# Optimization experiments

Measured on AMD Instinct MI355X. Metric: run time of the kernel, lower is better.

Reference implementation:

```python
import jax, jax.numpy as jnp
import numpy as np
from jax import lax

B, T = 32, 20
H, E, A, V = 256, 512, 256, 10000
GH, GW, D = 32, 32, 256          # info spatial grid and channel dim
P = GH * GW                      # num_pixels = 1024
IN_FLAT = P * D                  # 262144
REL = 128 * 128                  # 16384
LSTM_IN = E + D + H              # input to gate linears (x = [word, att_feat], then cat h)


def setup_inputs() -> dict:
    key = jax.random.key(0)
    ks = iter(jax.random.split(key, 40))
    def W(shape, scale=0.05):
        return jax.random.normal(next(ks), shape, jnp.float32) * scale
    inp = {}
    inp["info"] = jax.random.normal(next(ks), (B, GH, GW, D), jnp.float32)
    inp["relation"] = jax.random.normal(next(ks), (B, 128, 128), jnp.float32)
    inp["captions"] = jax.random.randint(next(ks), (B, T), 0, V)
    lens = jax.random.randint(next(ks), (B, 1), 5, T + 1).at[0, 0].set(T)
    inp["captions_lens"] = lens
    # embedding + attention
    inp["emb"] = W((V, E), 0.1)
    inp["W_enc"] = W((D, A)); inp["b_enc"] = jnp.zeros((A,), jnp.float32)
    inp["W_dec"] = W((H, A)); inp["b_dec"] = jnp.zeros((A,), jnp.float32)
    inp["W_full"] = W((A,));  inp["b_full"] = jnp.zeros((), jnp.float32)
    # MSLSTM cell (5 gate linears + mlp)
    for g in ("i", "f", "o", "g1", "g2"):
        inp[f"W_{g}"] = W((LSTM_IN, H)); inp[f"b_{g}"] = jnp.zeros((H,), jnp.float32)
    inp["W_mlp"] = W((2 * H, H)); inp["b_mlp"] = jnp.zeros((H,), jnp.float32)
    # f_beta, fc, init-state linears
    inp["W_beta"] = W((H, D)); inp["b_beta"] = jnp.zeros((D,), jnp.float32)
    inp["W_fc"] = W((H, V), 0.1); inp["b_fc"] = jnp.zeros((V,), jnp.float32)
    inp["W_ih"] = W((IN_FLAT, H), 0.005); inp["b_ih"] = jnp.zeros((H,), jnp.float32)
    inp["W_ic"] = W((IN_FLAT, H), 0.005); inp["b_ic"] = jnp.zeros((H,), jnp.float32)
    inp["W_iC"] = W((REL, H), 0.01);      inp["b_iC"] = jnp.zeros((H,), jnp.float32)
    return inp


def reference(info, relation, captions, captions_lens, emb,
              W_enc, b_enc, W_dec, b_dec, W_full, b_full,
              W_i, b_i, W_f, b_f, W_o, b_o, W_g1, b_g1, W_g2, b_g2,
              W_mlp, b_mlp, W_beta, b_beta, W_fc, b_fc,
              W_ih, b_ih, W_ic, b_ic, W_iC, b_iC):
    Bsz = captions.shape[0]
    info_f = info.reshape(Bsz, P, D)
    rel_f = relation.reshape(Bsz, REL)
    lens = captions_lens[:, 0]
    order = jnp.argsort(-lens)                      # sort descending by length
    lens = lens[order]
    caps = captions[order]
    info_f = info_f[order]
    rel_f = rel_f[order]
    sent_len = lens - 1
    Tm = captions.shape[1] - 1                      # static: max len forced to T in setup

    words = emb[caps]                               # (B, T, E)
    flat = info_f.reshape(Bsz, -1)                  # (B, P*D)
    h = flat @ W_ih + b_ih
    c = flat @ W_ic + b_ic
    C = rel_f @ W_iC + b_iC
    att1 = info_f @ W_enc + b_enc                   # (B, P, A) -- invariant over t

    def step(carry, xs):
        h, c, C = carry
        word, t = xs                                # word: (B, E)
        att2 = h @ W_dec + b_dec                    # (B, A)
        e = jax.nn.relu(att1 + att2[:, None, :]) @ W_full + b_full   # (B, P)
        alpha = jax.nn.softmax(e, axis=1)
        awf = jnp.einsum('bpd,bp->bd', info_f, alpha)                # (B, D)
        # note: gate=sigmoid(f_beta(h)) is computed in torch but its product is unused
        x = jnp.concatenate([word, awf, h], axis=1)  # cat([x, h]) with x=[word, awf]
        i = jax.nn.sigmoid(x @ W_i + b_i)
        f = jax.nn.sigmoid(x @ W_f + b_f)
        o = jax.nn.sigmoid(x @ W_o + b_o)
        g1 = jnp.tanh(x @ W_g1 + b_g1)
        g2 = jnp.tanh(x @ W_g2 + b_g2)
        new_c = f * c + i * g1
        new_C = f * C + i * g2
        new_h = o * jnp.tanh(jnp.concatenate([new_c, new_C], axis=1) @ W_mlp + b_mlp)
        pred = new_h @ W_fc + b_fc                  # dropout in eval mode = identity
        mask = (sent_len > t)[:, None].astype(pred.dtype)
        return (new_h, new_c, new_C), (pred * mask, alpha * mask)

    words_t = jnp.swapaxes(words[:, :Tm], 0, 1)     # (Tm, B, E)
    (_, (preds, alphas)) = lax.scan(step, (h, c, C), (words_t, jnp.arange(Tm)))
    predictions = jnp.swapaxes(preds, 0, 1)         # (B, Tm, V)
    alphas = jnp.swapaxes(alphas, 0, 1)             # (B, Tm, P)
    return predictions, alphas, order
```

## Files before the change

### kernel.cpp

```cpp
#include <hip/hip_runtime.h>
#include <math.h>

#define Bz 32
#define Tz 20
#define TMz 19
#define Vz 10000
#define INFLAT 262144
#define RELSZ 16384
#define NBLK 512

#define WS_PH     0
#define WS_PC     4194304
#define WS_ATT1H  0
#define WS_INFOH  4194304
#define WS_EXPE   8388608
#define WS_ZSUM   8421376
#define WS_AWF    8421888
#define WS_GSP    8430080
#define WS_HST    8593920
#define WS_CST0   8602112
#define WS_CSTB0  8610304
#define WS_CST1   8618496
#define WS_CSTB1  8626688
#define WS_AT2P   8634880
#define WS_INTS   8700416
#define WS_PCHC   8701440

__device__ __forceinline__ float sigm(float x) { return 1.0f / (1.0f + expf(-x)); }

__device__ __forceinline__ unsigned short f2bf(float f) {
    unsigned int x = __float_as_uint(f);
    unsigned int r = (x + 0x7fffu + ((x >> 16) & 1u)) >> 16;
    return (unsigned short)r;
}
__device__ __forceinline__ float bfl(unsigned int u) { return __uint_as_float(u << 16); }
__device__ __forceinline__ float bfh(unsigned int u) { return __uint_as_float(u & 0xffff0000u); }

__device__ __forceinline__ float agload(const float* p) {
    return __hip_atomic_load(p, __ATOMIC_RELAXED, __HIP_MEMORY_SCOPE_AGENT);
}
__device__ __forceinline__ void agstore(float* p, float v) {
    __hip_atomic_store(p, v, __ATOMIC_RELAXED, __HIP_MEMORY_SCOPE_AGENT);
}
__device__ __forceinline__ int agloadi(const int* p) {
    return __hip_atomic_load(p, __ATOMIC_RELAXED, __HIP_MEMORY_SCOPE_AGENT);
}
__device__ __forceinline__ void agstorei(int* p, int v) {
    __hip_atomic_store(p, v, __ATOMIC_RELAXED, __HIP_MEMORY_SCOPE_AGENT);
}
__device__ __forceinline__ void agadd(float* p, float v) {
    __hip_atomic_fetch_add(p, v, __ATOMIC_RELAXED, __HIP_MEMORY_SCOPE_AGENT);
}

__device__ __forceinline__ void gl_lds16(const float* g, float* l) {
    __builtin_amdgcn_global_load_lds(
        (const __attribute__((address_space(1))) unsigned int*)g,
        (__attribute__((address_space(3))) unsigned int*)l,
        16, 0, 0);
}

__device__ __forceinline__ void gbar(int* slots, int* root, int gen) {
    asm volatile("s_waitcnt vmcnt(0)" ::: "memory");
    __syncthreads();
    if (blockIdx.x == 0) {
        int i0 = threadIdx.x, i1 = threadIdx.x + 256;
        if (i0 != 0) {
            while (agloadi(&slots[i0]) < gen) __builtin_amdgcn_s_sleep(1);
        }
        while (agloadi(&slots[i1]) < gen) __builtin_amdgcn_s_sleep(1);
        __syncthreads();
        if (threadIdx.x == 0) agstorei(root, gen);
    } else if (threadIdx.x == 0) {
        agstorei(&slots[blockIdx.x], gen);
        while (agloadi(root) < gen) __builtin_amdgcn_s_sleep(2);
    }
    __syncthreads();
    asm volatile("" ::: "memory");
}

__global__ void k_sort(const int* __restrict__ lens, float* __restrict__ out_order,
                       int* __restrict__ ord, int* __restrict__ sentlen, int* __restrict__ barmem) {
    if (threadIdx.x == 0 && blockIdx.x == 0) {
        for (int i = 0; i < 64 + NBLK; ++i) barmem[i] = 0;
        int l[Bz]; bool used[Bz];
        for (int b = 0; b < Bz; ++b) { l[b] = lens[b]; used[b] = false; }
        for (int i = 0; i < Bz; ++i) {
            int best = -1;
            for (int j = 0; j < Bz; ++j)
                if (!used[j] && (best < 0 || l[j] > l[best])) best = j;
            used[best] = true;
            ord[i] = best;
            sentlen[i] = l[best] - 1;
            out_order[i] = (float)best;
        }
    }
}

__global__ __launch_bounds__(256) void k_gemv2(const float* __restrict__ X, const int* __restrict__ ord,
                                               const float* __restrict__ W1, const float* __restrict__ W2,
                                               float* __restrict__ p1, float* __restrict__ p2) {
    __shared__ __align__(16) float wlds[8192];
    __shared__ __align__(16) float xsT[256 * 36];
    __shared__ int ords[32];
    int tid = threadIdx.x;
    int wv = tid >> 6, ln = tid & 63;
    size_t k0 = (size_t)blockIdx.x * 512;

    if (tid < 32) ords[tid] = ord[tid];
    __syncthreads();

    auto stage_xs = [&](int hh) {
        for (int idx = tid; idx < 2048; idx += 256) {
            int b = idx >> 6, kq = idx & 63;
            float4 v = *(const float4*)&X[(size_t)ords[b] * INFLAT + k0 + (size_t)hh * 256 + kq * 4];
            xsT[(kq * 4 + 0) * 36 + b] = v.x;
            xsT[(kq * 4 + 1) * 36 + b] = v.y;
            xsT[(kq * 4 + 2) * 36 + b] = v.z;
            xsT[(kq * 4 + 3) * 36 + b] = v.w;
        }
    };
    auto issue = [&](int n) {
        int slot = n & 1;
        size_t krow = k0 + (size_t)n * 8 + wv * 2;
        const float* g1 = W1 + krow * 256 + ln * 4;
        const float* g2 = W2 + krow * 256 + ln * 4;
        float* l1 = &wlds[slot * 4096 + (wv * 2) * 256 + ln * 4];
        float* l2 = &wlds[slot * 4096 + 2048 + (wv * 2) * 256 + ln * 4];
        gl_lds16(g1, l1);
        gl_lds16(g2, l2);
        gl_lds16(g1 + 256, l1 + 256);
        gl_lds16(g2 + 256, l2 + 256);
    };

    float ah[32], ac[32];
#pragma unroll
    for (int b = 0; b < 32; ++b) { ah[b] = 0.f; ac[b] = 0.f; }

    stage_xs(0);
    issue(0);

#pragma unroll 1
    for (int c = 0; c < 64; ++c) {
        if (c == 32) stage_xs(1);
        if (c + 1 < 64) {
            issue(c + 1);
            asm volatile("s_waitcnt vmcnt(4)" ::: "memory");
        } else {
            asm volatile("s_waitcnt vmcnt(0)" ::: "memory");
        }
        __syncthreads();
        int slot = c & 1;
        int xb0 = (c & 31) * 8;
#pragma unroll
        for (int kk = 0; kk < 8; ++kk) {
            float w1 = wlds[slot * 4096 + kk * 256 + tid];
            float w2 = wlds[slot * 4096 + 2048 + kk * 256 + tid];
            const float4* xr = (const float4*)&xsT[(xb0 + kk) * 36];
#pragma unroll
            for (int bq = 0; bq < 8; ++bq) {
                float4 x4 = xr[bq];
                ah[bq * 4 + 0] += x4.x * w1; ac[bq * 4 + 0] += x4.x * w2;
                ah[bq * 4 + 1] += x4.y * w1; ac[bq * 4 + 1] += x4.y * w2;
                ah[bq * 4 + 2] += x4.z * w1; ac[bq * 4 + 2] += x4.z * w2;
                ah[bq * 4 + 3] += x4.w * w1; ac[bq * 4 + 3] += x4.w * w2;
            }
        }
        __syncthreads();
    }
#pragma unroll
    for (int b = 0; b < 32; ++b) {
        size_t o = ((size_t)blockIdx.x * 32 + b) * 256 + tid;
        p1[o] = ah[b];
        p2[o] = ac[b];
    }
}

__global__ __launch_bounds__(256) void k_gemvC(const float* __restrict__ R, const int* __restrict__ ord,
                                               const float* __restrict__ W, float* __restrict__ p) {
    __shared__ float xs[32 * 128];
    __shared__ int ords[32];
    int tid = threadIdx.x, bx = blockIdx.x;
    if (tid < 32) ords[tid] = ord[tid];
    __syncthreads();
    int k0 = bx * 128;
    for (int idx = tid; idx < 32 * 128; idx += 256) {
        int b = idx >> 7, kk = idx & 127;
        xs[idx] = R[(size_t)ords[b] * RELSZ + k0 + kk];
    }
    __syncthreads();
    float acc[32];
#pragma unroll
    for (int b = 0; b < 32; ++b) acc[b] = 0.f;
    for (int kk = 0; kk < 128; ++kk) {
        float w = W[(size_t)(k0 + kk) * 256 + tid];
#pragma unroll
        for (int b = 0; b < 32; ++b) acc[b] += xs[b * 128 + kk] * w;
    }
#pragma unroll
    for (int b = 0; b < 32; ++b) p[((size_t)bx * 32 + b) * 256 + tid] = acc[b];
}

__global__ __launch_bounds__(256) void k_reduce3(const float* __restrict__ ph, const float* __restrict__ pc,
                                                 const float* __restrict__ pC,
                                                 const float* __restrict__ b_ih, const float* __restrict__ b_ic,
                                                 const float* __restrict__ b_iC,
                                                 float* __restrict__ hst, float* __restrict__ cst,
                                                 float* __restrict__ Cst) {
    int which = blockIdx.x >> 5, b = blockIdx.x & 31, j = threadIdx.x;
    if (which == 0) {
        float s0 = b_ih[j], s1 = 0.f, s2 = 0.f, s3 = 0.f;
        for (int c = 0; c < 512; c += 4) {
            s0 += ph[((size_t)((c + 0) * 32 + b)) * 256 + j];
            s1 += ph[((size_t)((c + 1) * 32 + b)) * 256 + j];
            s2 += ph[((size_t)((c + 2) * 32 + b)) * 256 + j];
            s3 += ph[((size_t)((c + 3) * 32 + b)) * 256 + j];
        }
        hst[b * 256 + j] = s0 + s1 + s2 + s3;
    } else if (which == 1) {
        float s0 = b_ic[j], s1 = 0.f, s2 = 0.f, s3 = 0.f;
        for (int c = 0; c < 512; c += 4) {
            s0 += pc[((size_t)((c + 0) * 32 + b)) * 256 + j];
            s1 += pc[((size_t)((c + 1) * 32 + b)) * 256 + j];
            s2 += pc[((size_t)((c + 2) * 32 + b)) * 256 + j];
            s3 += pc[((size_t)((c + 3) * 32 + b)) * 256 + j];
        }
        cst[b * 256 + j] = s0 + s1 + s2 + s3;
    } else {
        float s0 = b_iC[j], s1 = 0.f, s2 = 0.f, s3 = 0.f;
        for (int c = 0; c < 128; c += 4) {
            s0 += pC[((size_t)((c + 0) * 32 + b)) * 256 + j];
            s1 += pC[((size_t)((c + 1) * 32 + b)) * 256 + j];
            s2 += pC[((size_t)((c + 2) * 32 + b)) * 256 + j];
            s3 += pC[((size_t)((c + 3) * 32 + b)) * 256 + j];
        }
        Cst[b * 256 + j] = s0 + s1 + s2 + s3;
    }
}

__global__ __launch_bounds__(256) void k_init2(const float* __restrict__ hst, const float* __restrict__ W_dec,
                                               float* __restrict__ at2p, float* __restrict__ awf,
                                               float* __restrict__ zsum) {
    __shared__ __align__(16) float hs[8192];
    int tid = threadIdx.x;
    for (int i = blockIdx.x * 256 + tid; i < 8192; i += 1024) awf[i] = 0.f;
    if (blockIdx.x == 0 && tid < 32) zsum[tid] = 0.f;
    for (int i = tid; i < 2048; i += 256) ((float4*)hs)[i] = ((const float4*)hst)[i];
    __syncthreads();
    int col = blockIdx.x * 64 + (tid & 63), bg = tid >> 6;
    float acc[8] = {0.f,0.f,0.f,0.f,0.f,0.f,0.f,0.f};
    for (int k = 0; k < 256; ++k) {
        float w = W_dec[(size_t)k * 256 + col];
#pragma unroll
        for (int bi = 0; bi < 8; ++bi) acc[bi] += hs[(bg * 8 + bi) * 256 + k] * w;
    }
#pragma unroll
    for (int bi = 0; bi < 8; ++bi) {
        int b = bg * 8 + bi;
        at2p[((size_t)(b * 8 + 0)) * 256 + col] = acc[bi];
#pragma unroll
        for (int ct = 1; ct < 8; ++ct) at2p[((size_t)(b * 8 + ct)) * 256 + col] = 0.f;
    }
}

__global__ __launch_bounds__(256) void k_att1(const float* __restrict__ info, const int* __restrict__ ord,
                                              const float* __restrict__ W, const float* __restrict__ bias,
                                              unsigned short* __restrict__ att1h,
                                              unsigned short* __restrict__ infoh) {
    __shared__ __align__(16) float xsT[256 * 36];
    int tid = threadIdx.x;
    int r0 = blockIdx.x * 32;
    int b = r0 >> 10, p0 = r0 & 1023;
    const float* src = info + (size_t)ord[b] * INFLAT + (size_t)p0 * 256;
    for (int idx = tid; idx < 2048; idx += 256) {
        int r = idx >> 6, kq = idx & 63;
        float4 v = *(const float4*)&src[r * 256 + kq * 4];
        xsT[(kq * 4 + 0) * 36 + r] = v.x;
        xsT[(kq * 4 + 1) * 36 + r] = v.y;
        xsT[(kq * 4 + 2) * 36 + r] = v.z;
        xsT[(kq * 4 + 3) * 36 + r] = v.w;
    }
    __syncthreads();
#pragma unroll 4
    for (int r = 0; r < 32; ++r)
        infoh[(size_t)(r0 + r) * 256 + tid] = f2bf(xsT[tid * 36 + r]);
    float acc[32];
#pragma unroll
    for (int r = 0; r < 32; ++r) acc[r] = 0.f;
    for (int k = 0; k < 256; ++k) {
        float w = W[k * 256 + tid];
        const float4* xr = (const float4*)&xsT[k * 36];
#pragma unroll
        for (int rq = 0; rq < 8; ++rq) {
            float4 x4 = xr[rq];
            acc[rq * 4 + 0] += x4.x * w;
            acc[rq * 4 + 1] += x4.y * w;
            acc[rq * 4 + 2] += x4.z * w;
            acc[rq * 4 + 3] += x4.w * w;
        }
    }
    float bj = bias[tid];
#pragma unroll
    for (int r = 0; r < 32; ++r)
        att1h[(size_t)(r0 + r) * 256 + tid] = f2bf(acc[r] + bj);
}

struct KArgs {
    const float *info, *emb, *W_dec, *b_dec, *W_full, *b_full;
    const float *W_i, *W_f, *W_o, *W_g1, *W_g2;
    const float *b_i, *b_f, *b_o, *b_g1, *b_g2;
    const float *W_mlp, *b_mlp, *W_fc, *b_fc;
    const int *caps;
    const unsigned short *att1h, *infoh;
    float *expe, *zsum, *awf, *gsp, *hst, *cst0, *Cst0, *cst1, *Cst1, *at2p;
    const int *ord, *slp;
    int *root, *slots;
    float *out_pred, *out_alpha;
};

__device__ void pred_task2(const KArgs& a, unsigned short* hb, int tile, int tm1) {
    int tid = threadIdx.x;
    for (int i = tid; i < 8192; i += 256) hb[i] = f2bf(agload(&a.hst[i]));
    __syncthreads();
    int col = tile * 64 + (tid & 63), bg = tid >> 6;
    if (col >= Vz) return;
    float acc[8] = {0.f, 0.f, 0.f, 0.f, 0.f, 0.f, 0.f, 0.f};
    for (int jq = 0; jq < 64; ++jq) {
        float w0 = a.W_fc[(size_t)(jq * 4 + 0) * Vz + col];
        float w1 = a.W_fc[(size_t)(jq * 4 + 1) * Vz + col];
        float w2 = a.W_fc[(size_t)(jq * 4 + 2) * Vz + col];
        float w3 = a.W_fc[(size_t)(jq * 4 + 3) * Vz + col];
#pragma unroll
        for (int bi = 0; bi < 8; ++bi) {
            uint2 u = *(const uint2*)&hb[(bg * 8 + bi) * 256 + jq * 4];
            acc[bi] += bfl(u.x) * w0 + bfh(u.x) * w1 + bfl(u.y) * w2 + bfh(u.y) * w3;
        }
    }
    float bv = a.b_fc[col];
#pragma unroll
    for (int bi = 0; bi < 8; ++bi) {
        int b = bg * 8 + bi;
        float r = (a.slp[b] > tm1) ? (acc[bi] + bv) : 0.f;
        a.out_pred[((size_t)b * TMz + tm1) * Vz + col] = r;
    }
}

__global__ __launch_bounds__(256, 2) void k_steps(KArgs a) {
    __shared__ __align__(16) unsigned char smem[81920];
    unsigned char* attB = smem;
    unsigned char* infB = smem + 32768;
    float* F = (float*)(smem + 65536);
    unsigned short* S16 = (unsigned short*)(smem + 65536);

    int bid = blockIdx.x, tid = threadIdx.x;
    int b = bid >> 4, sub = bid & 15;
    int gen = 0;

    {
        const unsigned short* ag = a.att1h + (size_t)(b * 1024 + sub * 64) * 256;
        const unsigned short* ig = a.infoh + (size_t)(b * 1024 + sub * 64) * 256;
        for (int idx = tid; idx < 2048; idx += 256) {
            int r = idx >> 5, qc = idx & 31;
            uint4 v = *(const uint4*)(ag + (size_t)r * 256 + qc * 8);
            *(uint4*)(attB + r * 512 + ((qc ^ (r & 7)) << 4)) = v;
            uint4 w2 = *(const uint4*)(ig + (size_t)r * 256 + qc * 8);
            *(uint4*)(infB + idx * 16) = w2;
        }
    }
    __syncthreads();

    for (int t = 0; t < TMz; ++t) {
        {
            float v = a.b_dec[tid];
#pragma unroll
            for (int ct = 0; ct < 8; ++ct) v += agload(&a.at2p[((size_t)(b * 8 + ct)) * 256 + tid]);
            F[tid] = v;
            F[256 + tid] = a.W_full[tid];
            __syncthreads();
            int pl = tid & 63, kq = tid >> 6;
            float part = 0.f;
#pragma unroll
            for (int q = 0; q < 8; ++q) {
                int c = kq * 8 + q;
                uint4 u = *(const uint4*)(attB + pl * 512 + ((c ^ (pl & 7)) << 4));
                const float* A = F + kq * 64 + q * 8;
                const float* W = F + 256 + kq * 64 + q * 8;
                part += fmaxf(bfl(u.x) + A[0], 0.f) * W[0];
                part += fmaxf(bfh(u.x) + A[1], 0.f) * W[1];
                part += fmaxf(bfl(u.y) + A[2], 0.f) * W[2];
                part += fmaxf(bfh(u.y) + A[3], 0.f) * W[3];
                part += fmaxf(bfl(u.z) + A[4], 0.f) * W[4];
                part += fmaxf(bfh(u.z) + A[5], 0.f) * W[5];
                part += fmaxf(bfl(u.w) + A[6], 0.f) * W[6];
                part += fmaxf(bfh(u.w) + A[7], 0.f) * W[7];
            }
            F[512 + kq * 64 + pl] = part;
            __syncthreads();
            if (tid < 64) {
                float e = F[512 + tid] + F[576 + tid] + F[640 + tid] + F[704 + tid] + a.b_full[0];
                float ex = expf(e);
                agstore(&a.expe[b * 1024 + sub * 64 + tid], ex);
                F[768 + tid] = ex;
                float s = ex;
                s += __shfl_down(s, 32); s += __shfl_down(s, 16); s += __shfl_down(s, 8);
                s += __shfl_down(s, 4);  s += __shfl_down(s, 2);  s += __shfl_down(s, 1);
                if (tid == 0) agadd(&a.zsum[b], s);
            }
            __syncthreads();
            int gg = tid >> 7, c2 = tid & 127;
            const unsigned char* ib = infB + gg * 512 + c2 * 4;
            const float* ex = F + 768;
            float a0 = 0.f, a1 = 0.f;
#pragma unroll
            for (int i = 0; i < 32; ++i) {
                unsigned int u = *(const unsigned int*)(ib + i * 1024);
                float ev = ex[i * 2 + gg];
                a0 += ev * bfl(u);
                a1 += ev * bfh(u);
            }
            F[832 + gg * 256 + c2 * 2]     = a0;
            F[832 + gg * 256 + c2 * 2 + 1] = a1;
            __syncthreads();
            agadd(&a.awf[b * 256 + tid], F[832 + tid] + F[1088 + tid]);
        }
        gbar(a.slots, a.root, ++gen);

        if (bid < 80) {
            int g = bid / 16, s16 = bid % 16;
            int ct = s16 >> 2, kc = s16 & 3;
            const float* Wg = (g == 0) ? a.W_i : (g == 1) ? a.W_f : (g == 2) ? a.W_o : (g == 3) ? a.W_g1 : a.W_g2;
            for (int idx = tid; idx < 8192; idx += 256) {
                int b2 = idx >> 8, kk = idx & 255;
                float v;
                if (kc == 0) {
                    int cap = a.caps[a.ord[b2] * Tz + t];
                    v = a.emb[(size_t)cap * 512 + kk];
                } else if (kc == 1) {
                    int cap = a.caps[a.ord[b2] * Tz + t];
                    v = a.emb[(size_t)cap * 512 + 256 + kk];
                } else if (kc == 2) {
                    v = agload(&a.awf[b2 * 256 + kk]);
                } else {
                    v = agload(&a.hst[b2 * 256 + kk]);
                }
                S16[idx] = f2bf(v);
            }
            __syncthreads();
            int col = ct * 64 + (tid & 63), bg = tid >> 6;
            float acc[8] = {0.f,0.f,0.f,0.f,0.f,0.f,0.f,0.f};
            int wbase = kc * 256;
            for (int kk = 0; kk < 256; kk += 4) {
                float w0 = Wg[(size_t)(wbase + kk + 0) * 256 + col];
                float w1 = Wg[(size_t)(wbase + kk + 1) * 256 + col];
                float w2 = Wg[(size_t)(wbase + kk + 2) * 256 + col];
                float w3 = Wg[(size_t)(wbase + kk + 3) * 256 + col];
#pragma unroll
                for (int bi = 0; bi < 8; ++bi) {
                    uint2 u = *(const uint2*)&S16[(bg * 8 + bi) * 256 + kk];
                    acc[bi] += bfl(u.x) * w0 + bfh(u.x) * w1 + bfl(u.y) * w2 + bfh(u.y) * w3;
                }
            }
            if (kc == 2) {
#pragma unroll
                for (int bi = 0; bi < 8; ++bi) {
                    float Z = agload(&a.zsum[bg * 8 + bi]);
                    acc[bi] *= (1.0f / Z);
                }
            }
#pragma unroll
            for (int bi = 0; bi < 8; ++bi)
                agstore(&a.gsp[((size_t)((g * 4 + kc) * 32 + bg * 8 + bi)) * 256 + col], acc[bi]);
        } else if (bid < 112) {
            int bb = bid - 80;
            float Z = agload(&a.zsum[bb]);
            float invZ = 1.0f / Z;
            float am = (a.slp[bb] > t) ? invZ : 0.f;
            float* oal = a.out_alpha + ((size_t)bb * TMz + t) * 1024;
            for (int p = tid; p < 1024; p += 256) oal[p] = agload(&a.expe[bb * 1024 + p]) * am;
        } else if (t > 0 && bid < 269) {
            pred_task2(a, S16, bid - 112, t - 1);
        }
        gbar(a.slots, a.root, ++gen);

        if (bid < 256) {
            int bb = bid >> 3, ct = bid & 7;
            int j = tid;
            const float* csOld = (t & 1) ? a.cst1 : a.cst0;
            const float* CsOld = (t & 1) ? a.Cst1 : a.Cst0;
            float* csNew = (t & 1) ? a.cst0 : a.cst1;
            float* CsNew = (t & 1) ? a.Cst0 : a.Cst1;
            float gs[5];
#pragma unroll
            for (int g = 0; g < 5; ++g) {
                float s = 0.f;
#pragma unroll
                for (int kc = 0; kc < 4; ++kc)
                    s += agload(&a.gsp[((size_t)((g * 4 + kc) * 32 + bb)) * 256 + j]);
                gs[g] = s;
            }
            gs[0] += a.b_i[j]; gs[1] += a.b_f[j]; gs[2] += a.b_o[j];
            gs[3] += a.b_g1[j]; gs[4] += a.b_g2[j];
            float iv = sigm(gs[0]), fv = sigm(gs[1]), ov = sigm(gs[2]);
            float g1 = tanhf(gs[3]), g2 = tanhf(gs[4]);
            float nc = fv * agload(&csOld[bb * 256 + j]) + iv * g1;
            float nC = fv * agload(&CsOld[bb * 256 + j]) + iv * g2;
            if (ct == 0) {
                agstore(&csNew[bb * 256 + j], nc);
                agstore(&CsNew[bb * 256 + j], nC);
            }
            if (ct == 1 && tid == 0) agstore(&a.zsum[bb], 0.f);
            F[j] = nc;
            F[256 + j] = nC;
            F[512 + j] = ov;
            __syncthreads();
            int colL = tid & 31, kth = tid >> 5;
            int col = ct * 32 + colL;
            float part = 0.f;
            const float* wm = a.W_mlp + col;
            for (int i = 0; i < 64; ++i) {
                int k = kth * 64 + i;
                part += F[k] * wm[(size_t)k * 256];
            }
            F[768 + colL * 9 + kth] = part;
            __syncthreads();
            if (tid < 32) {
                int c2 = ct * 32 + tid;
                float m = a.b_mlp[c2];
#pragma unroll
                for (int kk = 0; kk < 8; ++kk) m += F[768 + tid * 9 + kk];
                float hv = F[512 + c2] * tanhf(m);
                agstore(&a.hst[bb * 256 + c2], hv);
                F[1056 + tid] = hv;
                agstore(&a.awf[bb * 256 + c2], 0.f);
            }
            __syncthreads();
            float acc = 0.f;
            const float* wd = a.W_dec + (size_t)(ct * 32) * 256 + tid;
#pragma unroll
            for (int kk = 0; kk < 32; ++kk) acc += F[1056 + kk] * wd[(size_t)kk * 256];
            agstore(&a.at2p[((size_t)(bb * 8 + ct)) * 256 + tid], acc);
        }
        gbar(a.slots, a.root, ++gen);
    }

    if (bid >= 112 && bid < 269) pred_task2(a, S16, bid - 112, TMz - 1);
}

extern "C" void kernel_launch(void* const* d_in, const int* in_sizes, int n_in,
                              void* d_out, int out_size, void* d_ws, size_t ws_size,
                              hipStream_t stream) {
    const float* info  = (const float*)d_in[0];
    const float* rel   = (const float*)d_in[1];
    const int*   caps  = (const int*)d_in[2];
    const int*   lens  = (const int*)d_in[3];
    const float* emb   = (const float*)d_in[4];
    const float* W_enc = (const float*)d_in[5];
    const float* b_enc = (const float*)d_in[6];
    const float* W_dec = (const float*)d_in[7];
    const float* b_dec = (const float*)d_in[8];
    const float* W_full= (const float*)d_in[9];
    const float* b_full= (const float*)d_in[10];
    const float* W_i   = (const float*)d_in[11];
    const float* b_i   = (const float*)d_in[12];
    const float* W_f   = (const float*)d_in[13];
    const float* b_f   = (const float*)d_in[14];
    const float* W_o   = (const float*)d_in[15];
    const float* b_o   = (const float*)d_in[16];
    const float* W_g1  = (const float*)d_in[17];
    const float* b_g1  = (const float*)d_in[18];
    const float* W_g2  = (const float*)d_in[19];
    const float* b_g2  = (const float*)d_in[20];
    const float* W_mlp = (const float*)d_in[21];
    const float* b_mlp = (const float*)d_in[22];
    const float* W_fc  = (const float*)d_in[25];
    const float* b_fc  = (const float*)d_in[26];
    const float* W_ih  = (const float*)d_in[27];
    const float* b_ih  = (const float*)d_in[28];
    const float* W_ic  = (const float*)d_in[29];
    const float* b_ic  = (const float*)d_in[30];
    const float* W_iC  = (const float*)d_in[31];
    const float* b_iC  = (const float*)d_in[32];

    float* out = (float*)d_out;
    float* out_pred  = out;
    float* out_alpha = out + (size_t)Bz * TMz * Vz;
    float* out_order = out_alpha + (size_t)Bz * TMz * 1024;

    float* w = (float*)d_ws;
    float* ph   = w + WS_PH;
    float* pcp  = w + WS_PC;
    unsigned short* att1h = (unsigned short*)(w + WS_ATT1H);
    unsigned short* infoh = (unsigned short*)(w + WS_INFOH);
    float* expe = w + WS_EXPE;
    float* zsum = w + WS_ZSUM;
    float* awf  = w + WS_AWF;
    float* gsp  = w + WS_GSP;
    float* hst  = w + WS_HST;
    float* cst0 = w + WS_CST0;
    float* Cst0 = w + WS_CSTB0;
    float* cst1 = w + WS_CST1;
    float* Cst1 = w + WS_CSTB1;
    float* at2p = w + WS_AT2P;
    int*   ordp = (int*)(w + WS_INTS);
    int*   slp  = ordp + 32;
    int*   barmem = ordp + 64;
    float* pC   = w + WS_PCHC;

    k_sort<<<1, 64, 0, stream>>>(lens, out_order, ordp, slp, barmem);
    k_gemv2<<<512, 256, 0, stream>>>(info, ordp, W_ih, W_ic, ph, pcp);
    k_gemvC<<<128, 256, 0, stream>>>(rel, ordp, W_iC, pC);
    k_reduce3<<<96, 256, 0, stream>>>(ph, pcp, pC, b_ih, b_ic, b_iC, hst, cst0, Cst0);
    k_init2<<<4, 256, 0, stream>>>(hst, W_dec, at2p, awf, zsum);
    k_att1<<<1024, 256, 0, stream>>>(info, ordp, W_enc, b_enc, att1h, infoh);

    KArgs ka;
    ka.info = info; ka.emb = emb; ka.W_dec = W_dec; ka.b_dec = b_dec;
    ka.W_full = W_full; ka.b_full = b_full;
    ka.W_i = W_i; ka.W_f = W_f; ka.W_o = W_o; ka.W_g1 = W_g1; ka.W_g2 = W_g2;
    ka.b_i = b_i; ka.b_f = b_f; ka.b_o = b_o; ka.b_g1 = b_g1; ka.b_g2 = b_g2;
    ka.W_mlp = W_mlp; ka.b_mlp = b_mlp; ka.W_fc = W_fc; ka.b_fc = b_fc;
    ka.caps = caps;
    ka.att1h = att1h; ka.infoh = infoh;
    ka.expe = expe; ka.zsum = zsum; ka.awf = awf;
    ka.gsp = gsp; ka.hst = hst;
    ka.cst0 = cst0; ka.Cst0 = Cst0; ka.cst1 = cst1; ka.Cst1 = Cst1;
    ka.at2p = at2p;
    ka.ord = ordp; ka.slp = slp;
    ka.root = barmem; ka.slots = barmem + 64;
    ka.out_pred = out_pred; ka.out_alpha = out_alpha;

    k_steps<<<NBLK, 256, 0, stream>>>(ka);
}
```

Baseline: 2.183 ms.

## Vectorize FC prediction tiles and move alpha output to second step phase

The per-step vocabulary projection now has each thread compute 4 adjacent columns for 4 batch rows using float4 weight loads and float4 stores. This halves the number of prediction blocks needed per step. The alpha-output write moves from the first barrier phase into the second phase on otherwise idle blocks. The softmax denominator is double-buffered by step parity so it can still be read there after the next step's accumulation is reset. The aim is to shorten the critical first phase and improve memory coalescing, at the cost of more registers per thread and fewer blocks sharing the FC work.

```diff
diff --git a/kernel.cpp b/kernel.cpp
--- a/kernel.cpp
+++ b/kernel.cpp
@@ -239,11 +239,11 @@
 
 __global__ __launch_bounds__(256) void k_init2(const float* __restrict__ hst, const float* __restrict__ W_dec,
                                                float* __restrict__ at2p, float* __restrict__ awf,
-                                               float* __restrict__ zsum) {
+                                               float* __restrict__ zsum2) {
     __shared__ __align__(16) float hs[8192];
     int tid = threadIdx.x;
     for (int i = blockIdx.x * 256 + tid; i < 8192; i += 1024) awf[i] = 0.f;
-    if (blockIdx.x == 0 && tid < 32) zsum[tid] = 0.f;
+    if (blockIdx.x == 0 && tid < 64) zsum2[tid] = 0.f;
     for (int i = tid; i < 2048; i += 256) ((float4*)hs)[i] = ((const float4*)hst)[i];
     __syncthreads();
     int col = blockIdx.x * 64 + (tid & 63), bg = tid >> 6;
@@ -311,36 +311,44 @@
     const float *W_mlp, *b_mlp, *W_fc, *b_fc;
     const int *caps;
     const unsigned short *att1h, *infoh;
-    float *expe, *zsum, *awf, *gsp, *hst, *cst0, *Cst0, *cst1, *Cst1, *at2p;
+    float *expe, *zsum2, *awf, *gsp, *hst, *cst0, *Cst0, *cst1, *Cst1, *at2p;
     const int *ord, *slp;
     int *root, *slots;
     float *out_pred, *out_alpha;
 };
 
-__device__ void pred_task2(const KArgs& a, unsigned short* hb, int tile, int tm1) {
+__device__ void pred_task3(const KArgs& a, unsigned short* hb, int tile, int tm1) {
     int tid = threadIdx.x;
     for (int i = tid; i < 8192; i += 256) hb[i] = f2bf(agload(&a.hst[i]));
     __syncthreads();
-    int col = tile * 64 + (tid & 63), bg = tid >> 6;
-    if (col >= Vz) return;
-    float acc[8] = {0.f, 0.f, 0.f, 0.f, 0.f, 0.f, 0.f, 0.f};
-    for (int jq = 0; jq < 64; ++jq) {
-        float w0 = a.W_fc[(size_t)(jq * 4 + 0) * Vz + col];
-        float w1 = a.W_fc[(size_t)(jq * 4 + 1) * Vz + col];
-        float w2 = a.W_fc[(size_t)(jq * 4 + 2) * Vz + col];
-        float w3 = a.W_fc[(size_t)(jq * 4 + 3) * Vz + col];
-#pragma unroll
-        for (int bi = 0; bi < 8; ++bi) {
-            uint2 u = *(const uint2*)&hb[(bg * 8 + bi) * 256 + jq * 4];
-            acc[bi] += bfl(u.x) * w0 + bfh(u.x) * w1 + bfl(u.y) * w2 + bfh(u.y) * w3;
-        }
-    }
-    float bv = a.b_fc[col];
-#pragma unroll
-    for (int bi = 0; bi < 8; ++bi) {
-        int b = bg * 8 + bi;
-        float r = (a.slp[b] > tm1) ? (acc[bi] + bv) : 0.f;
-        a.out_pred[((size_t)b * TMz + tm1) * Vz + col] = r;
+    int col = tile * 128 + (tid & 31) * 4;
+    int bg = tid >> 5;
+    if (col + 3 >= Vz) return;
+    float acc[4][4] = {};
+    for (int r = 0; r < 256; r += 2) {
+        float4 wa = *(const float4*)&a.W_fc[(size_t)r * Vz + col];
+        float4 wb = *(const float4*)&a.W_fc[(size_t)(r + 1) * Vz + col];
+#pragma unroll
+        for (int bi = 0; bi < 4; ++bi) {
+            unsigned int u = *(const unsigned int*)&hb[(bg * 4 + bi) * 256 + r];
+            float hl = bfl(u), hh = bfh(u);
+            acc[bi][0] += hl * wa.x + hh * wb.x;
+            acc[bi][1] += hl * wa.y + hh * wb.y;
+            acc[bi][2] += hl * wa.z + hh * wb.z;
+            acc[bi][3] += hl * wa.w + hh * wb.w;
+        }
+    }
+    float4 bv = *(const float4*)&a.b_fc[col];
+#pragma unroll
+    for (int bi = 0; bi < 4; ++bi) {
+        int b = bg * 4 + bi;
+        bool on = (a.slp[b] > tm1);
+        float4 r4;
+        r4.x = on ? acc[bi][0] + bv.x : 0.f;
+        r4.y = on ? acc[bi][1] + bv.y : 0.f;
+        r4.z = on ? acc[bi][2] + bv.z : 0.f;
+        r4.w = on ? acc[bi][3] + bv.w : 0.f;
+        *(float4*)&a.out_pred[((size_t)b * TMz + tm1) * Vz + col] = r4;
     }
 }
 
@@ -403,7 +411,7 @@
                 float s = ex;
                 s += __shfl_down(s, 32); s += __shfl_down(s, 16); s += __shfl_down(s, 8);
                 s += __shfl_down(s, 4);  s += __shfl_down(s, 2);  s += __shfl_down(s, 1);
-                if (tid == 0) agadd(&a.zsum[b], s);
+                if (tid == 0) agadd(&a.zsum2[(t & 1) * 32 + b], s);
             }
             __syncthreads();
             int gg = tid >> 7, c2 = tid & 127;
@@ -462,22 +470,15 @@
             if (kc == 2) {
 #pragma unroll
                 for (int bi = 0; bi < 8; ++bi) {
-                    float Z = agload(&a.zsum[bg * 8 + bi]);
+                    float Z = agload(&a.zsum2[(t & 1) * 32 + bg * 8 + bi]);
                     acc[bi] *= (1.0f / Z);
                 }
             }
 #pragma unroll
             for (int bi = 0; bi < 8; ++bi)
                 agstore(&a.gsp[((size_t)((g * 4 + kc) * 32 + bg * 8 + bi)) * 256 + col], acc[bi]);
-        } else if (bid < 112) {
-            int bb = bid - 80;
-            float Z = agload(&a.zsum[bb]);
-            float invZ = 1.0f / Z;
-            float am = (a.slp[bb] > t) ? invZ : 0.f;
-            float* oal = a.out_alpha + ((size_t)bb * TMz + t) * 1024;
-            for (int p = tid; p < 1024; p += 256) oal[p] = agload(&a.expe[bb * 1024 + p]) * am;
-        } else if (t > 0 && bid < 269) {
-            pred_task2(a, S16, bid - 112, t - 1);
+        } else if (t > 0 && bid < 159) {
+            pred_task3(a, S16, bid - 80, t - 1);
         }
         gbar(a.slots, a.root, ++gen);
 
@@ -507,7 +508,7 @@
                 agstore(&csNew[bb * 256 + j], nc);
                 agstore(&CsNew[bb * 256 + j], nC);
             }
-            if (ct == 1 && tid == 0) agstore(&a.zsum[bb], 0.f);
+            if (ct == 1 && tid == 0) agstore(&a.zsum2[((t + 1) & 1) * 32 + bb], 0.f);
             F[j] = nc;
             F[256 + j] = nC;
             F[512 + j] = ov;
@@ -538,11 +539,18 @@
 #pragma unroll
             for (int kk = 0; kk < 32; ++kk) acc += F[1056 + kk] * wd[(size_t)kk * 256];
             agstore(&a.at2p[((size_t)(bb * 8 + ct)) * 256 + tid], acc);
+        } else if (bid < 288) {
+            int bb = bid - 256;
+            float Z = agload(&a.zsum2[(t & 1) * 32 + bb]);
+            float invZ = 1.0f / Z;
+            float am = (a.slp[bb] > t) ? invZ : 0.f;
+            float* oal = a.out_alpha + ((size_t)bb * TMz + t) * 1024;
+            for (int p = tid; p < 1024; p += 256) oal[p] = agload(&a.expe[bb * 1024 + p]) * am;
         }
         gbar(a.slots, a.root, ++gen);
     }
 
-    if (bid >= 112 && bid < 269) pred_task2(a, S16, bid - 112, TMz - 1);
+    if (bid >= 80 && bid < 159) pred_task3(a, S16, bid - 80, TMz - 1);
 }
 
 extern "C" void kernel_launch(void* const* d_in, const int* in_sizes, int n_in,
@@ -591,7 +599,7 @@
     unsigned short* att1h = (unsigned short*)(w + WS_ATT1H);
     unsigned short* infoh = (unsigned short*)(w + WS_INFOH);
     float* expe = w + WS_EXPE;
-    float* zsum = w + WS_ZSUM;
+    float* zsum2= w + WS_ZSUM;
     float* awf  = w + WS_AWF;
     float* gsp  = w + WS_GSP;
     float* hst  = w + WS_HST;
@@ -609,7 +617,7 @@
     k_gemv2<<<512, 256, 0, stream>>>(info, ordp, W_ih, W_ic, ph, pcp);
     k_gemvC<<<128, 256, 0, stream>>>(rel, ordp, W_iC, pC);
     k_reduce3<<<96, 256, 0, stream>>>(ph, pcp, pC, b_ih, b_ic, b_iC, hst, cst0, Cst0);
-    k_init2<<<4, 256, 0, stream>>>(hst, W_dec, at2p, awf, zsum);
+    k_init2<<<4, 256, 0, stream>>>(hst, W_dec, at2p, awf, zsum2);
     k_att1<<<1024, 256, 0, stream>>>(info, ordp, W_enc, b_enc, att1h, infoh);
 
     KArgs ka;
@@ -620,7 +628,7 @@
     ka.W_mlp = W_mlp; ka.b_mlp = b_mlp; ka.W_fc = W_fc; ka.b_fc = b_fc;
     ka.caps = caps;
     ka.att1h = att1h; ka.infoh = infoh;
-    ka.expe = expe; ka.zsum = zsum; ka.awf = awf;
+    ka.expe = expe; ka.zsum2 = zsum2; ka.awf = awf;
     ka.gsp = gsp; ka.hst = hst;
     ka.cst0 = cst0; ka.Cst0 = Cst0; ka.cst1 = cst1; ka.Cst1 = Cst1;
     ka.at2p = at2p;
```

Result: slower. 2.489 ms (+14.0%).
